# Kernel optimization log

Measured on AMD Instinct MI355X. Metric: run time of the kernel, lower is better.

The kernel has to match this reference:

```python
import jax, jax.numpy as jnp
import numpy as np

T, S, B, D, H, F, E = 1024, 1024, 4, 1024, 16, 4096, 8
HD = D // H
N = T * B                      # tokens entering MoE
CAP = 2 * N // E               # top-2 capacity per expert


def setup_inputs() -> dict:
    key = jax.random.key(0)
    ks = jax.random.split(key, 16)
    sc = 0.02
    rn = lambda k, shp, s=sc: jax.random.normal(k, shp, jnp.float32) * s
    return {
        "tgt": jax.random.normal(ks[0], (T, B, D), jnp.float32),
        "memory": jax.random.normal(ks[1], (S, B, D), jnp.float32),
        "sa_in_w": rn(ks[2], (3 * D, D)), "sa_in_b": jnp.zeros((3 * D,), jnp.float32),
        "sa_out_w": rn(ks[3], (D, D)), "sa_out_b": jnp.zeros((D,), jnp.float32),
        "ca_in_w": rn(ks[4], (3 * D, D)), "ca_in_b": jnp.zeros((3 * D,), jnp.float32),
        "ca_out_w": rn(ks[5], (D, D)), "ca_out_b": jnp.zeros((D,), jnp.float32),
        "ln1_g": jnp.ones((D,), jnp.float32), "ln1_b": jnp.zeros((D,), jnp.float32),
        "ln2_g": jnp.ones((D,), jnp.float32), "ln2_b": jnp.zeros((D,), jnp.float32),
        "ln3_g": jnp.ones((D,), jnp.float32), "ln3_b": jnp.zeros((D,), jnp.float32),
        "wg": rn(ks[6], (D, E)),
        "w1": rn(ks[7], (E, D, F)), "b1": jnp.zeros((E, F), jnp.float32),
        "w2": rn(ks[8], (E, F, D)), "b2": jnp.zeros((E, D), jnp.float32),
    }


def layer_norm(x, g, b, eps=1e-5):
    mu = jnp.mean(x, axis=-1, keepdims=True)
    var = jnp.var(x, axis=-1, keepdims=True)
    return (x - mu) * jax.lax.rsqrt(var + eps) * g + b


def mha(q_in, k_in, v_in, in_w, in_b, out_w, out_b):
    # q_in: [Tq,B,D], k_in/v_in: [Tk,B,D]; torch MultiheadAttention math (eval)
    wq, wk, wv = jnp.split(in_w, 3, axis=0)
    bq, bk, bv = jnp.split(in_b, 3)
    def heads(x, w, bias):
        y = x @ w.T + bias                       # [Tx,B,D]
        return y.reshape(x.shape[0], B, H, HD).transpose(1, 2, 0, 3)  # [B,H,Tx,hd]
    q, k, v = heads(q_in, wq, bq), heads(k_in, wk, bk), heads(v_in, wv, bv)
    scores = jnp.einsum('bhtd,bhsd->bhts', q, k) / np.sqrt(HD)
    attn = jax.nn.softmax(scores, axis=-1)
    o = jnp.einsum('bhts,bhsd->bhtd', attn, v)   # [B,H,Tq,hd]
    o = o.transpose(2, 0, 1, 3).reshape(q_in.shape[0], B, D)
    return o @ out_w.T + out_b


def moe_top2(x, wg, w1, b1, w2, b2):
    # x: [N,D]. Top-2 gating with capacity dispatch + grouped expert FFN.
    logits = x @ wg                               # [N,E]
    gates = jax.nn.softmax(logits, axis=-1)
    idx1 = jnp.argmax(gates, axis=-1)             # [N]
    m1 = jax.nn.one_hot(idx1, E, dtype=x.dtype)   # [N,E]
    gates_wo1 = jnp.where(m1 > 0, -jnp.inf, logits)
    idx2 = jnp.argmax(gates_wo1, axis=-1)
    m2 = jax.nn.one_hot(idx2, E, dtype=x.dtype)
    ar = jnp.arange(N)
    g1 = gates[ar, idx1]
    g2 = gates[ar, idx2]
    denom = g1 + g2 + 1e-9
    g1, g2 = g1 / denom, g2 / denom
    # positions within each expert buffer (first-come-first-serve, top1 before top2)
    pos1 = jnp.cumsum(m1, axis=0)[ar, idx1] - 1
    counts1 = jnp.sum(m1, axis=0)                 # [E]
    pos2 = jnp.cumsum(m2, axis=0)[ar, idx2] - 1 + counts1[idx2]
    keep1 = (pos1 < CAP).astype(x.dtype)
    keep2 = (pos2 < CAP).astype(x.dtype)
    p1 = jnp.clip(pos1, 0, CAP - 1).astype(jnp.int32)
    p2 = jnp.clip(pos2, 0, CAP - 1).astype(jnp.int32)
    buf = jnp.zeros((E, CAP, D), x.dtype)
    buf = buf.at[idx1, p1].add(x * keep1[:, None])
    buf = buf.at[idx2, p2].add(x * keep2[:, None])
    # grouped expert FFN: [E,CAP,D] -> [E,CAP,F] -> [E,CAP,D]
    h = jax.nn.relu(jnp.einsum('ecd,edf->ecf', buf, w1) + b1[:, None, :])
    eo = jnp.einsum('ecf,efd->ecd', h, w2) + b2[:, None, :]
    out = eo[idx1, p1] * (g1 * keep1)[:, None] + eo[idx2, p2] * (g2 * keep2)[:, None]
    return out


def reference(tgt, memory, sa_in_w, sa_in_b, sa_out_w, sa_out_b,
              ca_in_w, ca_in_b, ca_out_w, ca_out_b,
              ln1_g, ln1_b, ln2_g, ln2_b, ln3_g, ln3_b,
              wg, w1, b1, w2, b2):
    t2 = mha(tgt, tgt, tgt, sa_in_w, sa_in_b, sa_out_w, sa_out_b)
    x = layer_norm(tgt + t2, ln1_g, ln1_b)
    t2 = mha(x, memory, memory, ca_in_w, ca_in_b, ca_out_w, ca_out_b)
    x = layer_norm(x + t2, ln2_g, ln2_b)
    m = moe_top2(x.reshape(N, D), wg, w1, b1, w2, b2).reshape(T, B, D)
    x = layer_norm(x + m, ln3_g, ln3_b)
    return x
```

## Files before the change

kernel.cpp:

```cpp
#include <hip/hip_runtime.h>
#include <hip/hip_bf16.h>


typedef __bf16 bf16;
typedef __bf16 bf16x2 __attribute__((ext_vector_type(2)));
typedef __bf16 bf16x4 __attribute__((ext_vector_type(4)));
typedef __bf16 bf16x8 __attribute__((ext_vector_type(8)));
typedef float  f32x4  __attribute__((ext_vector_type(4)));

static_assert(sizeof(bf16) == 2, "bf16 size");

#define CAP_ 1024

#define GLOAD16(g, l)                                                  \
  __builtin_amdgcn_global_load_lds(                                    \
      (const __attribute__((address_space(1))) unsigned int*)(g),      \
      (__attribute__((address_space(3))) unsigned int*)(l), 16, 0, 0)

#define BAR() do { asm volatile("" ::: "memory"); __builtin_amdgcn_s_barrier(); asm volatile("" ::: "memory"); } while (0)

static const long OFF_WSAIN  = 0L;
static const long OFF_WSAOUT = 6291456L;
static const long OFF_WCAIN  = 8388608L;
static const long OFF_WCAOUT = 14680064L;
static const long OFF_BTGT   = 16777216L;
static const long OFF_BMEM   = 25165824L;
static const long OFF_QKV    = 33554432L;
static const long OFF_EO1    = 33554432L;
static const long OFF_KVCA   = OFF_QKV + 8388608L;
static const long OFF_VT     = 58720256L;
static const long OFF_AO     = 67108864L;
static const long OFF_PROJ   = 75497472L;
static const long OFF_X1     = 92274688L;
static const long OFF_X2     = 109051904L;
static const long OFF_SCORES = 125829120L;
static const long OFF_H      = OFF_SCORES + 67108864L;
static const long OFF_GATE   = 260046848L;
static const long OFF_E1   = OFF_GATE;
static const long OFF_E2   = OFF_GATE + 16384L;
static const long OFF_G1   = OFF_GATE + 32768L;
static const long OFF_G2   = OFF_GATE + 49152L;
static const long OFF_D1   = OFF_GATE + 65536L;
static const long OFF_D2   = OFF_GATE + 81920L;
static const long OFF_S1   = OFF_GATE + 98304L;
static const long OFF_S2   = OFF_GATE + 114688L;
static const long OFF_P2T  = OFF_GATE + 131072L;

__device__ __forceinline__ int xcd_swz(int bid, int nwg) {
  int q = nwg >> 3, r = nwg & 7;
  int xcd = bid & 7, idx = bid >> 3;
  return (xcd < r ? xcd * (q + 1) : r * (q + 1) + (xcd - r) * q) + idx;
}

__global__ __launch_bounds__(256) void k_f32_to_bf16(const float* __restrict__ in,
                                                     bf16* __restrict__ out, long n4) {
  long i = (long)blockIdx.x * 256 + threadIdx.x;
  if (i >= n4) return;
  float4 v = ((const float4*)in)[i];
  bf16x4 o = {(bf16)v.x, (bf16)v.y, (bf16)v.z, (bf16)v.w};
  ((bf16x4*)out)[i] = o;
}

__global__ __launch_bounds__(256) void k_zero16(float4* __restrict__ p, long n) {
  long i = (long)blockIdx.x * 256 + threadIdx.x;
  if (i < n) p[i] = make_float4(0.f, 0.f, 0.f, 0.f);
}

__global__ __launch_bounds__(256) void k_transpose_f32_bf16(const float* __restrict__ in,
                                                            bf16* __restrict__ out, int R, int C) {
  __shared__ float t[64][70];
  int z = blockIdx.z;
  long r0 = (long)blockIdx.y * 64, c0 = (long)blockIdx.x * 64;
  const float* ib = in + (long)z * R * C;
  bf16* ob = out + (long)z * R * C;
  int x = threadIdx.x, y = threadIdx.y;
  #pragma unroll
  for (int j = 0; j < 4; j++) {
    int sr = y + j * 16;
    float4 v = *(const float4*)&ib[(r0 + sr) * C + c0 + x * 4];
    t[sr][x * 4 + 0] = v.x; t[sr][x * 4 + 1] = v.y;
    t[sr][x * 4 + 2] = v.z; t[sr][x * 4 + 3] = v.w;
  }
  __syncthreads();
  #pragma unroll
  for (int j = 0; j < 4; j++) {
    int sc = y + j * 16;
    #pragma unroll
    for (int i = 0; i < 2; i++) {
      int sr = x * 2 + i * 32;
      bf16x2 o = {(bf16)t[sr][sc], (bf16)t[sr + 1][sc]};
      *(bf16x2*)&ob[(c0 + sc) * R + r0 + sr] = o;
    }
  }
}

__global__ __launch_bounds__(256) void k_extract_vt(const bf16* __restrict__ in,
                                                    bf16* __restrict__ out, long rs, long sb) {
  __shared__ bf16 t[64][66];
  int z = blockIdx.z;
  long r0 = (long)blockIdx.y * 64;
  const bf16* ib = in + (long)(z >> 4) * sb + (long)(z & 15) * 64;
  bf16* ob = out + (long)z * 64 * 1024;
  int x = threadIdx.x, y = threadIdx.y;
  #pragma unroll
  for (int i = y; i < 64; i += 4) t[i][x] = ib[(r0 + i) * rs + x];
  __syncthreads();
  #pragma unroll
  for (int i = y; i < 64; i += 4) ob[(long)i * 1024 + r0 + x] = t[x][i];
}

template <int BM, int BN, int WM, int WN, bool RELU, typename OutT>
__global__ __launch_bounds__(256) void k_gemm_nt(
    const bf16* __restrict__ A, const bf16* __restrict__ Bp,
    OutT* __restrict__ C, const float* __restrict__ bias,
    int K, long lda, long ldb, long ldc, float alpha, int zdiv,
    long sA1, long sA0, long sB1, long sB0, long sC1, long sC0,
    long sBias1, long sBias0) {
  constexpr int BK = 32;
  constexpr int WTM = BM / WM, WTN = BN / WN, MR = WTM / 16, NR = WTN / 16;
  constexpr int AISS = BM * BK / 2048;
  constexpr int BISS = BN * BK / 2048;
  __shared__ bf16 sa[BM * BK];
  __shared__ bf16 sb[BN * BK];
  const int nwg = gridDim.x * gridDim.y * gridDim.z;
  const int bid = blockIdx.x + gridDim.x * (blockIdx.y + gridDim.y * blockIdx.z);
  const int lid = xcd_swz(bid, nwg);
  const int bx = lid % gridDim.x;
  const int rem = lid / gridDim.x;
  const int by = rem % gridDim.y;
  const int z = rem / gridDim.y;
  const int zh = z / zdiv, zl = z - zh * zdiv;
  const bf16* Ab = A + zh * sA1 + zl * sA0 + (long)by * BM * lda;
  const bf16* Bb = Bp + zh * sB1 + zl * sB0 + (long)bx * BN * ldb;
  const int tid = threadIdx.x, lane = tid & 63, wid = tid >> 6;
  const int wm = wid / WN, wn = wid % WN;

  const int srow = tid >> 2;
  const int scol = (tid & 3) * 8;
  const bf16* aptr[AISS];
  bf16* aldst[AISS];
  #pragma unroll
  for (int i = 0; i < AISS; i++) {
    aptr[i] = Ab + (long)(srow + i * 64) * lda + scol;
    aldst[i] = &sa[i * 2048 + (wid << 9)];
  }
  const bf16* bptr[BISS];
  bf16* bldst[BISS];
  #pragma unroll
  for (int i = 0; i < BISS; i++) {
    bptr[i] = Bb + (long)(srow + i * 64) * ldb + scol;
    bldst[i] = &sb[i * 2048 + (wid << 9)];
  }

  f32x4 acc[MR][NR] = {};
  const int rA = wm * WTM + (lane & 15);
  const int rB = wn * WTN + (lane & 15);
  const int kk = (lane >> 4) * 8;

  for (int k0 = 0; k0 < K; k0 += BK) {
    #pragma unroll
    for (int i = 0; i < AISS; i++) GLOAD16(aptr[i] + k0, aldst[i]);
    #pragma unroll
    for (int i = 0; i < BISS; i++) GLOAD16(bptr[i] + k0, bldst[i]);
    __syncthreads();
    bf16x8 af[MR], bfr[NR];
    #pragma unroll
    for (int mi = 0; mi < MR; mi++) af[mi] = *(const bf16x8*)&sa[(rA + mi * 16) * BK + kk];
    #pragma unroll
    for (int ni = 0; ni < NR; ni++) bfr[ni] = *(const bf16x8*)&sb[(rB + ni * 16) * BK + kk];
    #pragma unroll
    for (int mi = 0; mi < MR; mi++)
      #pragma unroll
      for (int ni = 0; ni < NR; ni++)
        acc[mi][ni] = __builtin_amdgcn_mfma_f32_16x16x32_bf16(af[mi], bfr[ni], acc[mi][ni], 0, 0, 0);
    __syncthreads();
  }
  OutT* Cb = C + zh * sC1 + zl * sC0;
  const float* biasb = bias ? (bias + zh * sBias1 + zl * sBias0) : nullptr;
  const long rowBase = (long)by * BM + wm * WTM + ((lane >> 4) * 4);
  const long colBase = (long)bx * BN + wn * WTN + (lane & 15);
  #pragma unroll
  for (int mi = 0; mi < MR; mi++) {
    #pragma unroll
    for (int ni = 0; ni < NR; ni++) {
      long col = colBase + ni * 16;
      float bv = biasb ? biasb[col] : 0.f;
      #pragma unroll
      for (int r = 0; r < 4; r++) {
        long row = rowBase + mi * 16 + r;
        float v = acc[mi][ni][r] * alpha + bv;
        if (RELU) v = fmaxf(v, 0.f);
        Cb[row * ldc + col] = (OutT)v;
      }
    }
  }
}

template <bool RELU, typename OutT>
__global__ __launch_bounds__(512, 2) void k_gemm8p(
    const bf16* __restrict__ A, const bf16* __restrict__ Bp,
    OutT* __restrict__ C, const float* __restrict__ bias,
    int K, long lda, long ldb, long ldc, int zdiv,
    long sA1, long sA0, long sB1, long sB0, long sC1, long sC0, long sBias1) {
  __shared__ bf16 smem[65536];
  const int nwg = gridDim.x * gridDim.y * gridDim.z;
  const int bid = blockIdx.x + gridDim.x * (blockIdx.y + gridDim.y * blockIdx.z);
  const int lid = xcd_swz(bid, nwg);
  const int bx = lid % gridDim.x;
  const int rem = lid / gridDim.x;
  const int by = rem % gridDim.y;
  const int z = rem / gridDim.y;
  const int zh = z / zdiv, zl = z - zh * zdiv;
  const bf16* Ab = A + zh * sA1 + zl * sA0 + (long)by * 256 * lda;
  const bf16* Bb = Bp + zh * sB1 + zl * sB0 + (long)bx * 256 * ldb;
  const int tid = threadIdx.x, lane = tid & 63, wid = tid >> 6;
  const int wm = wid >> 2, wn = wid & 3;
  const int lane15 = lane & 15, grp = lane >> 4;
  const int s_r = (wid << 3) + (lane >> 3);
  const int s_k = ((lane & 7) ^ (lane >> 3)) << 3;
  const int ldst = wid << 9;
  const int in0 = (grp << 4) ^ ((lane & 7) << 4);
  const int in1 = (64 | (grp << 4)) ^ ((lane & 7) << 4);

  const int NT = K >> 6;
  f32x4 acc[8][4] = {};
  bf16x8 a[4][2], b[2][2][2];

  auto stageA = [&](int q, long k0p, int cb) {
    GLOAD16(Ab + (long)((q << 6) + s_r) * lda + k0p + s_k, &smem[cb + (q << 12) + ldst]);
  };
  auto stageB = [&](int q, long k0p, int cb) {
    GLOAD16(Bb + (long)((q << 6) + s_r) * ldb + k0p + s_k, &smem[cb + 16384 + (q << 12) + ldst]);
  };
  auto loadA = [&](int mh, int cb) {
    #pragma unroll
    for (int mi2 = 0; mi2 < 4; mi2++) {
      int r = wm * 128 + mh * 64 + mi2 * 16 + lane15;
      a[mi2][0] = *(const bf16x8*)&smem[cb + (r << 6) + (in0 >> 1)];
      a[mi2][1] = *(const bf16x8*)&smem[cb + (r << 6) + (in1 >> 1)];
    }
  };
  auto loadB = [&](int nh, int cb) {
    #pragma unroll
    for (int ni2 = 0; ni2 < 2; ni2++) {
      int c = wn * 64 + nh * 32 + ni2 * 16 + lane15;
      b[nh][ni2][0] = *(const bf16x8*)&smem[cb + 16384 + (c << 6) + (in0 >> 1)];
      b[nh][ni2][1] = *(const bf16x8*)&smem[cb + 16384 + (c << 6) + (in1 >> 1)];
    }
  };
  auto mfmaQ = [&](int mh, int nh) {
    __builtin_amdgcn_s_setprio(1);
    #pragma unroll
    for (int ks = 0; ks < 2; ks++)
      #pragma unroll
      for (int mi2 = 0; mi2 < 4; mi2++)
        #pragma unroll
        for (int ni2 = 0; ni2 < 2; ni2++)
          acc[mh * 4 + mi2][nh * 2 + ni2] = __builtin_amdgcn_mfma_f32_16x16x32_bf16(
              a[mi2][ks], b[nh][ni2][ks], acc[mh * 4 + mi2][nh * 2 + ni2], 0, 0, 0);
    __builtin_amdgcn_s_setprio(0);
  };

  #pragma unroll
  for (int q = 0; q < 4; q++) { stageA(q, 0, 0); stageB(q, 0, 0); }
  #pragma unroll
  for (int q = 0; q < 4; q++) { stageA(q, 64, 32768); stageB(q, 64, 32768); }
  asm volatile("s_waitcnt vmcnt(8)" ::: "memory");
  BAR();

  for (int t = 0; t < NT; t++) {
    const int cb = (t & 1) << 15;
    const long k0p = (long)(t + 2) << 6;
    const bool dostage = (t + 2) < NT;
    loadA(0, cb); loadB(0, cb);
    BAR(); mfmaQ(0, 0); BAR();
    loadB(1, cb);
    if (dostage) { stageA(0, k0p, cb); stageA(2, k0p, cb); }
    BAR(); mfmaQ(0, 1); BAR();
    loadA(1, cb);
    if (dostage) { stageB(0, k0p, cb); stageB(1, k0p, cb); }
    BAR(); mfmaQ(1, 1); BAR();
    if (dostage) {
      stageA(1, k0p, cb); stageA(3, k0p, cb);
      stageB(2, k0p, cb); stageB(3, k0p, cb);
      asm volatile("s_waitcnt vmcnt(8)" ::: "memory");
    } else if (t + 1 < NT) {
      asm volatile("s_waitcnt vmcnt(0)" ::: "memory");
    }
    BAR(); mfmaQ(1, 0); BAR();
  }

  OutT* Cb = C + zh * sC1 + zl * sC0;
  const float* biasb = bias ? (bias + zh * sBias1) : nullptr;
  const long rowBase = (long)by * 256 + wm * 128 + grp * 4;
  const long colBase = (long)bx * 256 + wn * 64 + lane15;
  #pragma unroll
  for (int mi = 0; mi < 8; mi++) {
    #pragma unroll
    for (int ni = 0; ni < 4; ni++) {
      long col = colBase + ni * 16;
      float bv = biasb ? biasb[col] : 0.f;
      #pragma unroll
      for (int r = 0; r < 4; r++) {
        long row = rowBase + mi * 16 + r;
        float v = acc[mi][ni][r] + bv;
        if (RELU) v = fmaxf(v, 0.f);
        Cb[row * ldc + col] = (OutT)v;
      }
    }
  }
}

__global__ __launch_bounds__(256) void k_flash(
    const bf16* __restrict__ q, const bf16* __restrict__ kk,
    const bf16* __restrict__ vt, bf16* __restrict__ ao,
    long qrs, long krs) {
  __shared__ bf16 kt[2][2048];
  __shared__ bf16 vtt[2][2048];
  __shared__ bf16 p_lds[4][32 * 72];
  const int nwg = gridDim.x * gridDim.y;
  const int bid = blockIdx.x + gridDim.x * blockIdx.y;
  const int lid = xcd_swz(bid, nwg);
  const int qt = lid & 7;
  const int bh = lid >> 3;
  const int b = bh >> 4, h = bh & 15;
  const int tid = threadIdx.x, lane = tid & 63, wid = tid >> 6;
  const int colLane = lane & 15, grp = lane >> 4;
  const bf16* qb = q + (qrs >> 2) * b + h * 64;
  const bf16* kb = kk + (krs >> 2) * b + h * 64;
  const bf16* vb = vt + (long)bh * 65536;

  bf16x8 qf[2][2];
  const int qrow0 = qt * 128 + wid * 32 + colLane;
  #pragma unroll
  for (int mi = 0; mi < 2; mi++)
    #pragma unroll
    for (int ks = 0; ks < 2; ks++)
      qf[mi][ks] = *(const bf16x8*)&qb[(long)(qrow0 + mi * 16) * qrs + ks * 32 + grp * 8];

  const int srow = tid >> 2;
  const int scol = (tid & 3) * 8;

  f32x4 oacc[2][4] = {};
  float m_[2][4], l_[2][4];
  #pragma unroll
  for (int mi = 0; mi < 2; mi++)
    #pragma unroll
    for (int r = 0; r < 4; r++) { m_[mi][r] = -INFINITY; l_[mi][r] = 0.f; }
  bf16* pl = &p_lds[wid][0];

  for (int s0 = 0; s0 < 1024; s0 += 64) {
    GLOAD16(&kb[(long)(s0 + srow) * krs + scol], &kt[0][wid << 9]);
    GLOAD16(&kb[(long)(s0 + srow) * krs + 32 + scol], &kt[1][wid << 9]);
    GLOAD16(&vb[(long)srow * 1024 + s0 + scol], &vtt[0][wid << 9]);
    GLOAD16(&vb[(long)srow * 1024 + s0 + 32 + scol], &vtt[1][wid << 9]);
    __syncthreads();

    f32x4 sacc[2][4] = {};
    bf16x8 kf[4][2];
    #pragma unroll
    for (int ni = 0; ni < 4; ni++)
      #pragma unroll
      for (int ks = 0; ks < 2; ks++)
        kf[ni][ks] = *(const bf16x8*)&kt[ks][(colLane + ni * 16) * 32 + grp * 8];
    #pragma unroll
    for (int ks = 0; ks < 2; ks++)
      #pragma unroll
      for (int mi = 0; mi < 2; mi++)
        #pragma unroll
        for (int ni = 0; ni < 4; ni++)
          sacc[mi][ni] = __builtin_amdgcn_mfma_f32_16x16x32_bf16(qf[mi][ks], kf[ni][ks], sacc[mi][ni], 0, 0, 0);

    float mnew[2][4], sc[2][4], psum[2][4];
    #pragma unroll
    for (int mi = 0; mi < 2; mi++)
      #pragma unroll
      for (int r = 0; r < 4; r++) {
        float vx = fmaxf(fmaxf(sacc[mi][0][r], sacc[mi][1][r]),
                         fmaxf(sacc[mi][2][r], sacc[mi][3][r])) * 0.125f;
        #pragma unroll
        for (int o = 1; o < 16; o <<= 1) vx = fmaxf(vx, __shfl_xor(vx, o));
        float mn = fmaxf(m_[mi][r], vx);
        sc[mi][r] = __expf(m_[mi][r] - mn);
        m_[mi][r] = mn; mnew[mi][r] = mn;
        l_[mi][r] *= sc[mi][r];
        psum[mi][r] = 0.f;
      }
    #pragma unroll
    for (int mi = 0; mi < 2; mi++)
      #pragma unroll
      for (int ni = 0; ni < 4; ni++)
        #pragma unroll
        for (int r = 0; r < 4; r++)
          oacc[mi][ni][r] *= sc[mi][r];
    #pragma unroll
    for (int mi = 0; mi < 2; mi++)
      #pragma unroll
      for (int ni = 0; ni < 4; ni++)
        #pragma unroll
        for (int r = 0; r < 4; r++) {
          float p = __expf(sacc[mi][ni][r] * 0.125f - mnew[mi][r]);
          psum[mi][r] += p;
          pl[(mi * 16 + grp * 4 + r) * 72 + ni * 16 + colLane] = (bf16)p;
        }
    #pragma unroll
    for (int mi = 0; mi < 2; mi++)
      #pragma unroll
      for (int r = 0; r < 4; r++) {
        float ps = psum[mi][r];
        #pragma unroll
        for (int o = 1; o < 16; o <<= 1) ps += __shfl_xor(ps, o);
        l_[mi][r] += ps;
      }

    bf16x8 pa[2][2], vf[4][2];
    #pragma unroll
    for (int mi = 0; mi < 2; mi++)
      #pragma unroll
      for (int ks = 0; ks < 2; ks++)
        pa[mi][ks] = *(const bf16x8*)&pl[(colLane + mi * 16) * 72 + ks * 32 + grp * 8];
    #pragma unroll
    for (int ni = 0; ni < 4; ni++)
      #pragma unroll
      for (int ks = 0; ks < 2; ks++)
        vf[ni][ks] = *(const bf16x8*)&vtt[ks][(colLane + ni * 16) * 32 + grp * 8];
    #pragma unroll
    for (int ks = 0; ks < 2; ks++)
      #pragma unroll
      for (int mi = 0; mi < 2; mi++)
        #pragma unroll
        for (int ni = 0; ni < 4; ni++)
          oacc[mi][ni] = __builtin_amdgcn_mfma_f32_16x16x32_bf16(pa[mi][ks], vf[ni][ks], oacc[mi][ni], 0, 0, 0);
    __syncthreads();
  }

  #pragma unroll
  for (int mi = 0; mi < 2; mi++)
    #pragma unroll
    for (int r = 0; r < 4; r++) {
      float inv = 1.f / l_[mi][r];
      int t = qt * 128 + wid * 32 + mi * 16 + grp * 4 + r;
      long n = (long)t * 4 + b;
      #pragma unroll
      for (int ni = 0; ni < 4; ni++)
        ao[n * 1024 + h * 64 + ni * 16 + colLane] = (bf16)(oacc[mi][ni][r] * inv);
    }
}

__global__ __launch_bounds__(256) void k_add_ln(const float* __restrict__ a, const float* __restrict__ b,
                                                const float* __restrict__ g, const float* __restrict__ be,
                                                float* __restrict__ out, bf16* __restrict__ outb) {
  long row = blockIdx.x;
  int tid = threadIdx.x;
  const float* pa = a + row * 1024;
  const float* pb = b + row * 1024;
  float v[4];
  float s = 0.f, sq = 0.f;
  #pragma unroll
  for (int i = 0; i < 4; i++) {
    int c = tid + i * 256;
    float x = pa[c] + pb[c];
    v[i] = x; s += x; sq += x * x;
  }
  #pragma unroll
  for (int o = 32; o; o >>= 1) { s += __shfl_xor(s, o); sq += __shfl_xor(sq, o); }
  __shared__ float r1[4], r2[4];
  int wid = tid >> 6;
  if ((tid & 63) == 0) { r1[wid] = s; r2[wid] = sq; }
  __syncthreads();
  s = r1[0] + r1[1] + r1[2] + r1[3];
  sq = r2[0] + r2[1] + r2[2] + r2[3];
  float mu = s * (1.f / 1024.f);
  float var = sq * (1.f / 1024.f) - mu * mu;
  float rstd = rsqrtf(var + 1e-5f);
  #pragma unroll
  for (int i = 0; i < 4; i++) {
    int c = tid + i * 256;
    float y = (v[i] - mu) * rstd * g[c] + be[c];
    out[row * 1024 + c] = y;
    if (outb) outb[row * 1024 + c] = (bf16)y;
  }
}

__global__ __launch_bounds__(256) void k_gate(const float* __restrict__ x, const float* __restrict__ wg,
                                              int* __restrict__ e1, int* __restrict__ e2,
                                              float* __restrict__ g1, float* __restrict__ g2) {
  int n = blockIdx.x * 4 + (threadIdx.x >> 6);
  int lane = threadIdx.x & 63;
  const float* xr = x + (long)n * 1024;
  float acc[8] = {0.f, 0.f, 0.f, 0.f, 0.f, 0.f, 0.f, 0.f};
  for (int i = 0; i < 16; i++) {
    float xv = xr[i * 64 + lane];
    const float* wr = wg + (long)(i * 64 + lane) * 8;
    #pragma unroll
    for (int e = 0; e < 8; e++) acc[e] += xv * wr[e];
  }
  #pragma unroll
  for (int e = 0; e < 8; e++)
    #pragma unroll
    for (int o = 32; o; o >>= 1) acc[e] += __shfl_xor(acc[e], o);
  if (lane == 0) {
    int i1 = 0; float b1v = acc[0];
    #pragma unroll
    for (int e = 1; e < 8; e++) if (acc[e] > b1v) { b1v = acc[e]; i1 = e; }
    int i2 = -1; float b2v = -INFINITY;
    #pragma unroll
    for (int e = 0; e < 8; e++) if (e != i1 && acc[e] > b2v) { b2v = acc[e]; i2 = e; }
    float den = 0.f;
    #pragma unroll
    for (int e = 0; e < 8; e++) den += __expf(acc[e] - b1v);
    float gg1 = 1.f / den;
    float gg2 = __expf(b2v - b1v) / den;
    float dn = gg1 + gg2 + 1e-9f;
    e1[n] = i1; e2[n] = i2; g1[n] = gg1 / dn; g2[n] = gg2 / dn;
  }
}

__global__ __launch_bounds__(64) void k_positions(const int* __restrict__ e1, const int* __restrict__ e2,
                                                  const float* __restrict__ g1, const float* __restrict__ g2,
                                                  int* __restrict__ d1, int* __restrict__ d2,
                                                  float* __restrict__ s1, float* __restrict__ s2,
                                                  int* __restrict__ p2t) {
  const int lane = threadIdx.x;
  int base1[8] = {0, 0, 0, 0, 0, 0, 0, 0};
  int base2[8] = {0, 0, 0, 0, 0, 0, 0, 0};
  const unsigned long long lt = (1ull << lane) - 1ull;
  int na = e1[lane], nb = e2[lane];
  for (int c = 0; c < 64; c++) {
    int a = na, b = nb;
    if (c < 63) { na = e1[(c + 1) * 64 + lane]; nb = e2[(c + 1) * 64 + lane]; }
    int n = c * 64 + lane;
    int pa = 0, pb = 0;
    #pragma unroll
    for (int e = 0; e < 8; e++) {
      unsigned long long ba = __ballot(a == e);
      unsigned long long bb = __ballot(b == e);
      if (a == e) pa = base1[e] + __popcll(ba & lt);
      if (b == e) pb = base2[e] + __popcll(bb & lt);
      base1[e] += __popcll(ba);
      base2[e] += __popcll(bb);
    }
    d1[n] = a * CAP_ + (pa < CAP_ ? pa : CAP_ - 1);
    s1[n] = (pa < CAP_) ? g1[n] : 0.f;
    p2t[n] = pb;
  }
  __shared__ int c1[8];
  if (lane == 0) {
    c1[0] = base1[0]; c1[1] = base1[1]; c1[2] = base1[2]; c1[3] = base1[3];
    c1[4] = base1[4]; c1[5] = base1[5]; c1[6] = base1[6]; c1[7] = base1[7];
  }
  __syncthreads();
  for (int c = 0; c < 64; c++) {
    int n = c * 64 + lane;
    int b = e2[n];
    int pb = p2t[n] + c1[b];
    d2[n] = b * CAP_ + (pb < CAP_ ? pb : CAP_ - 1);
    s2[n] = (pb < CAP_) ? g2[n] : 0.f;
  }
}

__global__ __launch_bounds__(256) void k_scatter(const float* __restrict__ x, const int* __restrict__ d1,
                                                 const int* __restrict__ d2, const float* __restrict__ s1,
                                                 const float* __restrict__ s2, bf16* __restrict__ buf) {
  int n = blockIdx.x;
  int tid = threadIdx.x;
  const float* xr = x + (long)n * 1024;
  float v[4];
  #pragma unroll
  for (int i = 0; i < 4; i++) v[i] = xr[tid + i * 256];
  if (s1[n] != 0.f) {
    bf16* o = buf + (long)d1[n] * 1024;
    #pragma unroll
    for (int i = 0; i < 4; i++) o[tid + i * 256] = (bf16)v[i];
  }
  if (s2[n] != 0.f) {
    bf16* o = buf + (long)d2[n] * 1024;
    #pragma unroll
    for (int i = 0; i < 4; i++) o[tid + i * 256] = (bf16)v[i];
  }
}

__global__ __launch_bounds__(256) void k_gather_ln(const float* __restrict__ x,
                                                   const float* __restrict__ p0, const float* __restrict__ p1,
                                                   const float* __restrict__ b2,
                                                   const int* __restrict__ d1, const int* __restrict__ d2,
                                                   const float* __restrict__ s1, const float* __restrict__ s2,
                                                   const float* __restrict__ g, const float* __restrict__ be,
                                                   float* __restrict__ out) {
  long n = blockIdx.x;
  int tid = threadIdx.x;
  float a1 = s1[n], a2 = s2[n];
  long i1 = (long)d1[n] * 1024, i2 = (long)d2[n] * 1024;
  long e1b = (long)(d1[n] >> 10) * 1024, e2b = (long)(d2[n] >> 10) * 1024;
  const float* xr = x + n * 1024;
  float v[4];
  float s = 0.f, sq = 0.f;
  #pragma unroll
  for (int i = 0; i < 4; i++) {
    int c = tid + i * 256;
    float r1v = p0[i1 + c] + p1[i1 + c] + b2[e1b + c];
    float r2v = p0[i2 + c] + p1[i2 + c] + b2[e2b + c];
    float y = xr[c] + a1 * r1v + a2 * r2v;
    v[i] = y; s += y; sq += y * y;
  }
  #pragma unroll
  for (int o = 32; o; o >>= 1) { s += __shfl_xor(s, o); sq += __shfl_xor(sq, o); }
  __shared__ float r1[4], r2[4];
  int wid = tid >> 6;
  if ((tid & 63) == 0) { r1[wid] = s; r2[wid] = sq; }
  __syncthreads();
  s = r1[0] + r1[1] + r1[2] + r1[3];
  sq = r2[0] + r2[1] + r2[2] + r2[3];
  float mu = s * (1.f / 1024.f);
  float var = sq * (1.f / 1024.f) - mu * mu;
  float rstd = rsqrtf(var + 1e-5f);
  #pragma unroll
  for (int i = 0; i < 4; i++) {
    int c = tid + i * 256;
    out[n * 1024 + c] = (v[i] - mu) * rstd * g[c] + be[c];
  }
}

extern "C" void kernel_launch(void* const* d_in, const int* in_sizes, int n_in,
                              void* d_out, int out_size, void* d_ws, size_t ws_size,
                              hipStream_t stream) {
  const float* tgt      = (const float*)d_in[0];
  const float* memory   = (const float*)d_in[1];
  const float* sa_in_w  = (const float*)d_in[2];
  const float* sa_in_b  = (const float*)d_in[3];
  const float* sa_out_w = (const float*)d_in[4];
  const float* sa_out_b = (const float*)d_in[5];
  const float* ca_in_w  = (const float*)d_in[6];
  const float* ca_in_b  = (const float*)d_in[7];
  const float* ca_out_w = (const float*)d_in[8];
  const float* ca_out_b = (const float*)d_in[9];
  const float* ln1_g    = (const float*)d_in[10];
  const float* ln1_b    = (const float*)d_in[11];
  const float* ln2_g    = (const float*)d_in[12];
  const float* ln2_b    = (const float*)d_in[13];
  const float* ln3_g    = (const float*)d_in[14];
  const float* ln3_b    = (const float*)d_in[15];
  const float* wg       = (const float*)d_in[16];
  const float* w1       = (const float*)d_in[17];
  const float* b1       = (const float*)d_in[18];
  const float* w2       = (const float*)d_in[19];
  const float* b2       = (const float*)d_in[20];

  char* ws = (char*)d_ws;
  auto B16 = [&](long o) { return (bf16*)(ws + o); };
  auto F32 = [&](long o) { return (float*)(ws + o); };
  auto I32 = [&](long o) { return (int*)(ws + o); };

  const dim3 blk256(256), blk512(512), blkT16(16, 16), blkT(64, 4);

  k_f32_to_bf16<<<3072, blk256, 0, stream>>>(sa_in_w, B16(OFF_WSAIN), 3072L * 1024 / 4);
  k_f32_to_bf16<<<1024, blk256, 0, stream>>>(sa_out_w, B16(OFF_WSAOUT), 1024L * 1024 / 4);
  k_f32_to_bf16<<<3072, blk256, 0, stream>>>(ca_in_w, B16(OFF_WCAIN), 3072L * 1024 / 4);
  k_f32_to_bf16<<<1024, blk256, 0, stream>>>(ca_out_w, B16(OFF_WCAOUT), 1024L * 1024 / 4);
  k_f32_to_bf16<<<4096, blk256, 0, stream>>>(tgt, B16(OFF_BTGT), 4096L * 1024 / 4);
  k_f32_to_bf16<<<4096, blk256, 0, stream>>>(memory, B16(OFF_BMEM), 4096L * 1024 / 4);

  k_gemm_nt<128, 128, 2, 2, false, bf16><<<dim3(24, 32, 1), blk256, 0, stream>>>(
      B16(OFF_BTGT), B16(OFF_WSAIN), B16(OFF_QKV), sa_in_b,
      1024, 1024, 1024, 3072, 1.f, 1, 0, 0, 0, 0, 0, 0, 0, 0);
  k_extract_vt<<<dim3(1, 16, 64), blkT, 0, stream>>>(B16(OFF_QKV) + 2048, B16(OFF_VT), 12288, 3072);
  k_flash<<<dim3(8, 64), blk256, 0, stream>>>(
      B16(OFF_QKV), B16(OFF_QKV) + 1024, B16(OFF_VT), B16(OFF_AO), 12288, 12288);
  k_gemm_nt<128, 64, 4, 1, false, float><<<dim3(16, 32, 1), blk256, 0, stream>>>(
      B16(OFF_AO), B16(OFF_WSAOUT), F32(OFF_PROJ), sa_out_b,
      1024, 1024, 1024, 1024, 1.f, 1, 0, 0, 0, 0, 0, 0, 0, 0);
  k_add_ln<<<4096, blk256, 0, stream>>>(tgt, F32(OFF_PROJ), ln1_g, ln1_b, F32(OFF_X1), B16(OFF_BTGT));

  k_gemm_nt<128, 64, 4, 1, false, bf16><<<dim3(16, 32, 1), blk256, 0, stream>>>(
      B16(OFF_BTGT), B16(OFF_WCAIN), B16(OFF_QKV), ca_in_b,
      1024, 1024, 1024, 1024, 1.f, 1, 0, 0, 0, 0, 0, 0, 0, 0);
  k_gemm_nt<128, 64, 4, 1, false, bf16><<<dim3(32, 32, 1), blk256, 0, stream>>>(
      B16(OFF_BMEM), B16(OFF_WCAIN) + 1024L * 1024, B16(OFF_KVCA), ca_in_b + 1024,
      1024, 1024, 1024, 2048, 1.f, 1, 0, 0, 0, 0, 0, 0, 0, 0);
  k_extract_vt<<<dim3(1, 16, 64), blkT, 0, stream>>>(B16(OFF_KVCA) + 1024, B16(OFF_VT), 8192, 2048);
  k_flash<<<dim3(8, 64), blk256, 0, stream>>>(
      B16(OFF_QKV), B16(OFF_KVCA), B16(OFF_VT), B16(OFF_AO), 4096, 8192);
  k_gemm_nt<128, 64, 4, 1, false, float><<<dim3(16, 32, 1), blk256, 0, stream>>>(
      B16(OFF_AO), B16(OFF_WCAOUT), F32(OFF_PROJ), ca_out_b,
      1024, 1024, 1024, 1024, 1.f, 1, 0, 0, 0, 0, 0, 0, 0, 0);
  k_add_ln<<<4096, blk256, 0, stream>>>(F32(OFF_X1), F32(OFF_PROJ), ln2_g, ln2_b, F32(OFF_X2), (bf16*)nullptr);

  k_gate<<<1024, blk256, 0, stream>>>(F32(OFF_X2), wg, I32(OFF_E1), I32(OFF_E2), F32(OFF_G1), F32(OFF_G2));
  k_positions<<<1, 64, 0, stream>>>(I32(OFF_E1), I32(OFF_E2), F32(OFF_G1), F32(OFF_G2),
                                    I32(OFF_D1), I32(OFF_D2), F32(OFF_S1), F32(OFF_S2), I32(OFF_P2T));
  k_zero16<<<4096, blk256, 0, stream>>>((float4*)B16(OFF_QKV), 1048576L);
  k_scatter<<<4096, blk256, 0, stream>>>(F32(OFF_X2), I32(OFF_D1), I32(OFF_D2),
                                         F32(OFF_S1), F32(OFF_S2), B16(OFF_QKV));
  k_transpose_f32_bf16<<<dim3(64, 16, 8), blkT16, 0, stream>>>(w1, B16(OFF_SCORES), 1024, 4096);
  k_gemm8p<true, bf16><<<dim3(16, 4, 8), blk512, 0, stream>>>(
      B16(OFF_QKV), B16(OFF_SCORES), B16(OFF_H), b1,
      1024, 1024, 1024, 4096, 1,
      1048576, 0, 4194304, 0, 4194304, 0, 4096);
  k_transpose_f32_bf16<<<dim3(16, 64, 8), blkT16, 0, stream>>>(w2, B16(OFF_SCORES), 4096, 1024);
  k_gemm8p<false, float><<<dim3(4, 4, 16), blk512, 0, stream>>>(
      B16(OFF_H), B16(OFF_SCORES), F32(OFF_PROJ), nullptr,
      2048, 4096, 4096, 1024, 2,
      4194304, 2048, 4194304, 2048, 1048576, (OFF_EO1 - OFF_PROJ) / 4, 0);
  k_gather_ln<<<4096, blk256, 0, stream>>>(F32(OFF_X2), F32(OFF_PROJ), F32(OFF_EO1), b2,
                                           I32(OFF_D1), I32(OFF_D2),
                                           F32(OFF_S1), F32(OFF_S2), ln3_g, ln3_b, (float*)d_out);

  (void)in_sizes; (void)n_in; (void)out_size; (void)ws_size;
}
```

Before: 636.2 us.

## Fuse input conversions, restage GEMM epilogue via LDS, use 256x256 GEMM for QKV

Merges six separate fp32-to-bf16 conversion launches into one kernel that picks its source and destination by block index. The 256x256 GEMM now keeps precomputed per-row global pointers and advances them each K step instead of recomputing addresses. Its epilogue stages accumulators through shared memory so it can issue wide, coalesced row stores instead of scattered scalar ones. The self-attention QKV projection switches from the 128x128 tiled GEMM to this 512-thread, 256x256 kernel. The epilogue adds barriers and LDS traffic, and the larger tile yields only 192 workgroups for the QKV projection.

```diff
diff --git a/kernel.cpp b/kernel.cpp
--- a/kernel.cpp
+++ b/kernel.cpp
@@ -52,13 +52,24 @@
   return (xcd < r ? xcd * (q + 1) : r * (q + 1) + (xcd - r) * q) + idx;
 }
 
-__global__ __launch_bounds__(256) void k_f32_to_bf16(const float* __restrict__ in,
-                                                     bf16* __restrict__ out, long n4) {
-  long i = (long)blockIdx.x * 256 + threadIdx.x;
-  if (i >= n4) return;
-  float4 v = ((const float4*)in)[i];
+__global__ __launch_bounds__(256) void k_cvt6(
+    const float* __restrict__ s0, const float* __restrict__ s1,
+    const float* __restrict__ s2, const float* __restrict__ s3,
+    const float* __restrict__ s4, const float* __restrict__ s5,
+    bf16* __restrict__ d0, bf16* __restrict__ d1, bf16* __restrict__ d2,
+    bf16* __restrict__ d3, bf16* __restrict__ d4, bf16* __restrict__ d5) {
+  long b = blockIdx.x;
+  const float* s; bf16* d; long off;
+  if (b < 3072)       { s = s0; d = d0; off = b; }
+  else if (b < 4096)  { s = s1; d = d1; off = b - 3072; }
+  else if (b < 7168)  { s = s2; d = d2; off = b - 4096; }
+  else if (b < 8192)  { s = s3; d = d3; off = b - 7168; }
+  else if (b < 12288) { s = s4; d = d4; off = b - 8192; }
+  else                { s = s5; d = d5; off = b - 12288; }
+  long i = off * 256 + threadIdx.x;
+  float4 v = ((const float4*)s)[i];
   bf16x4 o = {(bf16)v.x, (bf16)v.y, (bf16)v.z, (bf16)v.w};
-  ((bf16x4*)out)[i] = o;
+  ((bf16x4*)d)[i] = o;
 }
 
 __global__ __launch_bounds__(256) void k_zero16(float4* __restrict__ p, long n) {
@@ -226,12 +237,14 @@
   f32x4 acc[8][4] = {};
   bf16x8 a[4][2], b[2][2][2];
 
-  auto stageA = [&](int q, long k0p, int cb) {
-    GLOAD16(Ab + (long)((q << 6) + s_r) * lda + k0p + s_k, &smem[cb + (q << 12) + ldst]);
-  };
-  auto stageB = [&](int q, long k0p, int cb) {
-    GLOAD16(Bb + (long)((q << 6) + s_r) * ldb + k0p + s_k, &smem[cb + 16384 + (q << 12) + ldst]);
-  };
+  const bf16* pA[4];
+  const bf16* pB[4];
+  #pragma unroll
+  for (int q = 0; q < 4; q++) {
+    pA[q] = Ab + (long)((q << 6) + s_r) * lda + s_k;
+    pB[q] = Bb + (long)((q << 6) + s_r) * ldb + s_k;
+  }
+
   auto loadA = [&](int mh, int cb) {
     #pragma unroll
     for (int mi2 = 0; mi2 < 4; mi2++) {
@@ -262,51 +275,92 @@
   };
 
   #pragma unroll
-  for (int q = 0; q < 4; q++) { stageA(q, 0, 0); stageB(q, 0, 0); }
-  #pragma unroll
-  for (int q = 0; q < 4; q++) { stageA(q, 64, 32768); stageB(q, 64, 32768); }
+  for (int q = 0; q < 4; q++) {
+    GLOAD16(pA[q], &smem[(q << 12) + ldst]);
+    GLOAD16(pB[q], &smem[16384 + (q << 12) + ldst]);
+  }
+  #pragma unroll
+  for (int q = 0; q < 4; q++) {
+    GLOAD16(pA[q] + 64, &smem[32768 + (q << 12) + ldst]);
+    GLOAD16(pB[q] + 64, &smem[32768 + 16384 + (q << 12) + ldst]);
+  }
   asm volatile("s_waitcnt vmcnt(8)" ::: "memory");
   BAR();
 
   for (int t = 0; t < NT; t++) {
     const int cb = (t & 1) << 15;
-    const long k0p = (long)(t + 2) << 6;
     const bool dostage = (t + 2) < NT;
     loadA(0, cb); loadB(0, cb);
     BAR(); mfmaQ(0, 0); BAR();
     loadB(1, cb);
-    if (dostage) { stageA(0, k0p, cb); stageA(2, k0p, cb); }
+    if (dostage) {
+      GLOAD16(pA[0] + 128, &smem[cb + ldst]);
+      GLOAD16(pA[2] + 128, &smem[cb + (2 << 12) + ldst]);
+    }
     BAR(); mfmaQ(0, 1); BAR();
     loadA(1, cb);
-    if (dostage) { stageB(0, k0p, cb); stageB(1, k0p, cb); }
+    if (dostage) {
+      GLOAD16(pB[0] + 128, &smem[cb + 16384 + ldst]);
+      GLOAD16(pB[1] + 128, &smem[cb + 16384 + (1 << 12) + ldst]);
+    }
     BAR(); mfmaQ(1, 1); BAR();
     if (dostage) {
-      stageA(1, k0p, cb); stageA(3, k0p, cb);
-      stageB(2, k0p, cb); stageB(3, k0p, cb);
+      GLOAD16(pA[1] + 128, &smem[cb + (1 << 12) + ldst]);
+      GLOAD16(pA[3] + 128, &smem[cb + (3 << 12) + ldst]);
+      GLOAD16(pB[2] + 128, &smem[cb + 16384 + (2 << 12) + ldst]);
+      GLOAD16(pB[3] + 128, &smem[cb + 16384 + (3 << 12) + ldst]);
       asm volatile("s_waitcnt vmcnt(8)" ::: "memory");
     } else if (t + 1 < NT) {
       asm volatile("s_waitcnt vmcnt(0)" ::: "memory");
     }
     BAR(); mfmaQ(1, 0); BAR();
-  }
-
+    #pragma unroll
+    for (int q = 0; q < 4; q++) { pA[q] += 64; pB[q] += 64; }
+  }
+
+  float* eb = (float*)smem;
+  constexpr int EPS = 264;
+  const float* biasb = bias ? (bias + zh * sBias1) : nullptr;
+  float bv[4];
+  #pragma unroll
+  for (int ni = 0; ni < 4; ni++)
+    bv[ni] = biasb ? biasb[(long)bx * 256 + wn * 64 + ni * 16 + lane15] : 0.f;
   OutT* Cb = C + zh * sC1 + zl * sC0;
-  const float* biasb = bias ? (bias + zh * sBias1) : nullptr;
-  const long rowBase = (long)by * 256 + wm * 128 + grp * 4;
-  const long colBase = (long)bx * 256 + wn * 64 + lane15;
+  const int err = tid >> 4;
+  const int ecc = (tid & 15) << 4;
+  const long grB = (long)by * 256 + (err < 16 ? err : 112 + err);
+  const long gcB = (long)bx * 256 + ecc;
+  const int wrow = wm * 16 + grp * 4;
+  const int wcol = wn * 64 + lane15;
   #pragma unroll
   for (int mi = 0; mi < 8; mi++) {
+    BAR();
     #pragma unroll
     for (int ni = 0; ni < 4; ni++) {
-      long col = colBase + ni * 16;
-      float bv = biasb ? biasb[col] : 0.f;
       #pragma unroll
       for (int r = 0; r < 4; r++) {
-        long row = rowBase + mi * 16 + r;
-        float v = acc[mi][ni][r] + bv;
+        float v = acc[mi][ni][r] + bv[ni];
         if (RELU) v = fmaxf(v, 0.f);
-        Cb[row * ldc + col] = (OutT)v;
+        eb[(wrow + r) * EPS + wcol + ni * 16] = v;
       }
+    }
+    BAR();
+    float4 vv[4];
+    #pragma unroll
+    for (int j = 0; j < 4; j++)
+      vv[j] = *(const float4*)&eb[err * EPS + ecc + j * 4];
+    long grow = grB + mi * 16;
+    if constexpr (sizeof(OutT) == 2) {
+      bf16x8 o0 = {(bf16)vv[0].x, (bf16)vv[0].y, (bf16)vv[0].z, (bf16)vv[0].w,
+                   (bf16)vv[1].x, (bf16)vv[1].y, (bf16)vv[1].z, (bf16)vv[1].w};
+      bf16x8 o1 = {(bf16)vv[2].x, (bf16)vv[2].y, (bf16)vv[2].z, (bf16)vv[2].w,
+                   (bf16)vv[3].x, (bf16)vv[3].y, (bf16)vv[3].z, (bf16)vv[3].w};
+      *(bf16x8*)&Cb[grow * ldc + gcB] = o0;
+      *(bf16x8*)&Cb[grow * ldc + gcB + 8] = o1;
+    } else {
+      #pragma unroll
+      for (int j = 0; j < 4; j++)
+        *(float4*)&Cb[grow * ldc + gcB + j * 4] = vv[j];
     }
   }
 }
@@ -653,16 +707,13 @@
 
   const dim3 blk256(256), blk512(512), blkT16(16, 16), blkT(64, 4);
 
-  k_f32_to_bf16<<<3072, blk256, 0, stream>>>(sa_in_w, B16(OFF_WSAIN), 3072L * 1024 / 4);
-  k_f32_to_bf16<<<1024, blk256, 0, stream>>>(sa_out_w, B16(OFF_WSAOUT), 1024L * 1024 / 4);
-  k_f32_to_bf16<<<3072, blk256, 0, stream>>>(ca_in_w, B16(OFF_WCAIN), 3072L * 1024 / 4);
-  k_f32_to_bf16<<<1024, blk256, 0, stream>>>(ca_out_w, B16(OFF_WCAOUT), 1024L * 1024 / 4);
-  k_f32_to_bf16<<<4096, blk256, 0, stream>>>(tgt, B16(OFF_BTGT), 4096L * 1024 / 4);
-  k_f32_to_bf16<<<4096, blk256, 0, stream>>>(memory, B16(OFF_BMEM), 4096L * 1024 / 4);
-
-  k_gemm_nt<128, 128, 2, 2, false, bf16><<<dim3(24, 32, 1), blk256, 0, stream>>>(
+  k_cvt6<<<16384, blk256, 0, stream>>>(sa_in_w, sa_out_w, ca_in_w, ca_out_w, tgt, memory,
+                                       B16(OFF_WSAIN), B16(OFF_WSAOUT), B16(OFF_WCAIN),
+                                       B16(OFF_WCAOUT), B16(OFF_BTGT), B16(OFF_BMEM));
+
+  k_gemm8p<false, bf16><<<dim3(12, 16, 1), blk512, 0, stream>>>(
       B16(OFF_BTGT), B16(OFF_WSAIN), B16(OFF_QKV), sa_in_b,
-      1024, 1024, 1024, 3072, 1.f, 1, 0, 0, 0, 0, 0, 0, 0, 0);
+      1024, 1024, 1024, 3072, 1, 0, 0, 0, 0, 0, 0, 0);
   k_extract_vt<<<dim3(1, 16, 64), blkT, 0, stream>>>(B16(OFF_QKV) + 2048, B16(OFF_VT), 12288, 3072);
   k_flash<<<dim3(8, 64), blk256, 0, stream>>>(
       B16(OFF_QKV), B16(OFF_QKV) + 1024, B16(OFF_VT), B16(OFF_AO), 12288, 12288);
```

Measured after the change: 641.8 us. Within noise of the previous version (+0.9%).
